# Kernel optimization log

Hardware: AMD Instinct MI355X
Metric: run time of the kernel (lower is better)

The kernel has to match this reference:

```python
import jax, jax.numpy as jnp
from jax import lax
import numpy as np

H = 32  # hidden size
I = 1   # input size

def setup_inputs() -> dict:
    key = jax.random.key(0)
    ks = jax.random.split(key, 8)
    B, T = 4096, 512
    s_ih = 1.0 / np.sqrt(H)
    inp = {
        "x": jax.random.normal(ks[0], (B, T, I), dtype=jnp.float32),
        # PyTorch LSTM params, gate order (i, f, g, o)
        "W_ih": jax.random.uniform(ks[1], (4 * H, I), dtype=jnp.float32, minval=-s_ih, maxval=s_ih),
        "W_hh": jax.random.uniform(ks[2], (4 * H, H), dtype=jnp.float32, minval=-s_ih, maxval=s_ih),
        "b_ih": jax.random.uniform(ks[3], (4 * H,), dtype=jnp.float32, minval=-s_ih, maxval=s_ih),
        "b_hh": jax.random.uniform(ks[4], (4 * H,), dtype=jnp.float32, minval=-s_ih, maxval=s_ih),
        "W_head": jax.random.uniform(ks[5], (1, H), dtype=jnp.float32, minval=-s_ih, maxval=s_ih),
        "b_head": jax.random.uniform(ks[6], (1,), dtype=jnp.float32, minval=-s_ih, maxval=s_ih),
    }
    return inp

def reference(x, W_ih, W_hh, b_ih, b_hh, W_head, b_head):
    B, T, _ = x.shape
    # Precompute input contribution to all gates: [B, T, 4H]
    x_gates = jnp.einsum('bti,gi->btg', x, W_ih) + b_ih + b_hh

    def step(carry, xg_t):  # xg_t: [B, 4H]
        h, c = carry
        gates = xg_t + h @ W_hh.T
        i, f, g, o = jnp.split(gates, 4, axis=-1)
        i = jax.nn.sigmoid(i)
        f = jax.nn.sigmoid(f)
        g = jnp.tanh(g)
        o = jax.nn.sigmoid(o)
        c = f * c + i * g
        h = o * jnp.tanh(c)
        return (h, c), None

    h0 = jnp.zeros((B, H), dtype=x.dtype)
    c0 = jnp.zeros((B, H), dtype=x.dtype)
    (h_last, _), _ = lax.scan(step, (h0, c0), jnp.swapaxes(x_gates, 0, 1))
    # head on last timestep: [B, 1]
    return h_last @ W_head.T + b_head
```

## Files before the change

### kernel.cpp

```cpp
#include <hip/hip_runtime.h>

#define HID 32
#define SEQ 512
#define WAVES_PER_BLOCK 8
#define BLOCK (WAVES_PER_BLOCK * 64)

typedef float v2f __attribute__((ext_vector_type(2)));


#define GRP(WA, WB, WC, WD, HP) \
  "v_pk_fma_f32 v[80:81], v[" WA "], " HP ", v[80:81] op_sel_hi:[1,0,1]\n\t" \
  "v_pk_fma_f32 v[82:83], v[" WC "], " HP ", v[82:83] op_sel_hi:[1,0,1]\n\t" \
  "v_pk_fma_f32 v[80:81], v[" WB "], " HP ", v[80:81] op_sel:[0,1,0] op_sel_hi:[1,1,1]\n\t" \
  "v_pk_fma_f32 v[82:83], v[" WD "], " HP ", v[82:83] op_sel:[0,1,0] op_sel_hi:[1,1,1]\n\t"

#define CLOBS \
  "v64","v65","v66","v67","v68","v69","v70","v71","v72","v73","v74","v75", \
  "v76","v77","v78","v79","v80","v81","v82","v83","v84","v85","v86","v87", \
  "v88","v89","v90","v91","v92","v93","v94","v95","v96","v97","v98","v99", \
  "v100","v101","v102","v103","v104","v105","v106","v107","v108","v109", \
  "v110","v111","v112","v113","v114","v115","v116","v117","v118","v119", \
  "v120","v121","v122","v123","v124","v125","v126","v127","v128","v129", \
  "v130","v131","v132","v133","v134","v135","v136","v137","v138","v139", \
  "v140","v141","v142","v143","v144","v145","v146","v147","v148","v149", \
  "v150","v151","v152","v153","v154","v155","v156","v157","v158","v159", \
  "v160","v161","v162","v163","v164","v165","v166","v167","v168","v169", \
  "v170","v171","v172","v173","v174","v175","v176","v177","v178","v179", \
  "v180","v181","v182","v183","v184","v185","v186","v187","v188","v189", \
  "v190","v191","v192","v193","v194","v195","v196","v197","v198","v199", \
  "v200","v201","v202","v203","v204","v205","v206","v207","v208","v209", \
  "v210","v211","v212","v213","v214","v215","v216","v217","v218","v219", \
  "v220","v221","v222","v223","v224","v225","v226","v227","v228","v229", \
  "v230","v231","v232","v233","v234","v235","v236","v237","v238","v239"

#define MAC_ASM(XA) \
    asm volatile( \
        "ds_read2_b32 v[84:85], %[xa] offset0:0 offset1:0\n\t" \
        "ds_read_b128 v[64:67],   %[hr] offset:0\n\t" \
        "ds_read_b128 v[68:71],   %[hr] offset:16\n\t" \
        "ds_read_b128 v[72:75],   %[hr] offset:32\n\t" \
        "ds_read_b128 v[76:79],   %[hr] offset:48\n\t" \
        "ds_read_b128 v[224:227], %[hr] offset:64\n\t" \
        "ds_read_b128 v[228:231], %[hr] offset:80\n\t" \
        "ds_read_b128 v[232:235], %[hr] offset:96\n\t" \
        "ds_read_b128 v[236:239], %[hr] offset:112\n\t" \
        "v_add_u32 %[xa], 4, %[xa]\n\t" \
        "s_waitcnt lgkmcnt(8)\n\t" \
        "v_pk_fma_f32 v[80:81], %[uvIF], v[84:85], %[bvIF]\n\t" \
        "v_pk_fma_f32 v[82:83], %[uvGO], v[84:85], %[bvGO]\n\t" \
        "s_waitcnt lgkmcnt(7)\n\t" \
        GRP("96:97","98:99","160:161","162:163","v[64:65]") \
        GRP("100:101","102:103","164:165","166:167","v[66:67]") \
        "s_waitcnt lgkmcnt(6)\n\t" \
        GRP("104:105","106:107","168:169","170:171","v[68:69]") \
        GRP("108:109","110:111","172:173","174:175","v[70:71]") \
        "s_waitcnt lgkmcnt(5)\n\t" \
        GRP("112:113","114:115","176:177","178:179","v[72:73]") \
        GRP("116:117","118:119","180:181","182:183","v[74:75]") \
        "s_waitcnt lgkmcnt(4)\n\t" \
        GRP("120:121","122:123","184:185","186:187","v[76:77]") \
        GRP("124:125","126:127","188:189","190:191","v[78:79]") \
        "s_waitcnt lgkmcnt(3)\n\t" \
        GRP("128:129","130:131","192:193","194:195","v[224:225]") \
        GRP("132:133","134:135","196:197","198:199","v[226:227]") \
        "s_waitcnt lgkmcnt(2)\n\t" \
        GRP("136:137","138:139","200:201","202:203","v[228:229]") \
        GRP("140:141","142:143","204:205","206:207","v[230:231]") \
        "s_waitcnt lgkmcnt(1)\n\t" \
        GRP("144:145","146:147","208:209","210:211","v[232:233]") \
        GRP("148:149","150:151","212:213","214:215","v[234:235]") \
        "s_waitcnt lgkmcnt(0)\n\t" \
        GRP("152:153","154:155","216:217","218:219","v[236:237]") \
        GRP("156:157","158:159","220:221","222:223","v[238:239]") \
        : [xa]"+v"(XA) \
        : [hr]"v"(hr), [uvIF]"v"(uvIF), [bvIF]"v"(bvIF), \
          [uvGO]"v"(uvGO), [bvGO]"v"(bvGO) \
        : "memory", CLOBS)

#define ACT_ASM() \
    asm volatile( \
        "v_mul_f32 v86, 0xbfb8aa3b, v80\n\t" \
        "v_mul_f32 v87, 0xbfb8aa3b, v81\n\t" \
        "v_mul_f32 v88, 0x4038aa3b, v82\n\t" \
        "v_mul_f32 v89, 0xbfb8aa3b, v83\n\t" \
        "v_exp_f32 v86, v86\n\t" \
        "v_exp_f32 v87, v87\n\t" \
        "v_exp_f32 v88, v88\n\t" \
        "v_exp_f32 v89, v89\n\t" \
        "v_add_f32 v86, 1.0, v86\n\t" \
        "v_add_f32 v87, 1.0, v87\n\t" \
        "v_add_f32 v88, 1.0, v88\n\t" \
        "v_add_f32 v89, 1.0, v89\n\t" \
        "v_rcp_f32 v86, v86\n\t" \
        "v_rcp_f32 v87, v87\n\t" \
        "v_rcp_f32 v88, v88\n\t" \
        "v_rcp_f32 v89, v89\n\t" \
        "s_nop 1\n\t" \
        "v_fma_f32 v90, -2.0, v88, 1.0\n\t" \
        "v_mul_f32 v91, v86, v90\n\t" \
        "v_fma_f32 %[c], v87, %[c], v91\n\t" \
        "v_mul_f32 v92, 0x4038aa3b, %[c]\n\t" \
        "v_exp_f32 v92, v92\n\t" \
        "s_nop 1\n\t" \
        "v_add_f32 v92, 1.0, v92\n\t" \
        "v_rcp_f32 v92, v92\n\t" \
        "s_nop 1\n\t" \
        "v_fma_f32 v92, -2.0, v92, 1.0\n\t" \
        "v_mul_f32 %[h], v89, v92\n\t" \
        "ds_write_b32 %[hw], %[h]\n\t" \
        : [h]"+v"(h), [c]"+v"(c) \
        : [hw]"v"(hw) \
        : "memory", CLOBS)

#define BAR() __builtin_amdgcn_s_barrier()

__global__ __launch_bounds__(BLOCK)
void lstm_fused_kernel(
    const float* __restrict__ x,
    const float* __restrict__ W_ih,
    const float* __restrict__ W_hh,
    const float* __restrict__ b_ih,
    const float* __restrict__ b_hh,
    const float* __restrict__ W_head,
    const float* __restrict__ b_head,
    float* __restrict__ out)
{
    __shared__ __align__(16) v2f WIFL[32][34];
    __shared__ __align__(16) v2f WGOL[32][34];
    __shared__ __align__(16) float Xall[WAVES_PER_BLOCK][2][SEQ];
    __shared__ __align__(16) float Hbuf[WAVES_PER_BLOCK][2][32];

    const int tid = threadIdx.x;
    for (int idx = tid; idx < 1024; idx += BLOCK) {
        const int u = idx >> 5;
        const int j = idx & 31;
        WIFL[u][j] = (v2f){ W_hh[u * 32 + j],        W_hh[(32 + u) * 32 + j] };
        WGOL[u][j] = (v2f){ W_hh[(64 + u) * 32 + j], W_hh[(96 + u) * 32 + j] };
    }
    {
        const int base = blockIdx.x * 16;
        for (int idx = tid; idx < 16 * SEQ; idx += BLOCK) {
            const int smp = idx >> 9;
            const int t   = idx & (SEQ - 1);
            Xall[smp >> 1][smp & 1][t] = x[(size_t)(base + smp) * SEQ + t];
        }
    }
    __syncthreads();

    const int lane = tid & 63;
    const int u    = lane & 31;
    const int s    = lane >> 5;
    const int wid  = tid >> 6;
    const bool even = (wid < 4);

    {
        const unsigned aIF = (unsigned)(size_t)&WIFL[u][0];
        const unsigned aGO = (unsigned)(size_t)&WGOL[u][0];
        asm volatile(
            "ds_read_b128 v[96:99],   %[wa] offset:0\n\t"
            "ds_read_b128 v[100:103], %[wa] offset:16\n\t"
            "ds_read_b128 v[104:107], %[wa] offset:32\n\t"
            "ds_read_b128 v[108:111], %[wa] offset:48\n\t"
            "ds_read_b128 v[112:115], %[wa] offset:64\n\t"
            "ds_read_b128 v[116:119], %[wa] offset:80\n\t"
            "ds_read_b128 v[120:123], %[wa] offset:96\n\t"
            "ds_read_b128 v[124:127], %[wa] offset:112\n\t"
            "ds_read_b128 v[128:131], %[wa] offset:128\n\t"
            "ds_read_b128 v[132:135], %[wa] offset:144\n\t"
            "ds_read_b128 v[136:139], %[wa] offset:160\n\t"
            "ds_read_b128 v[140:143], %[wa] offset:176\n\t"
            "ds_read_b128 v[144:147], %[wa] offset:192\n\t"
            "ds_read_b128 v[148:151], %[wa] offset:208\n\t"
            "ds_read_b128 v[152:155], %[wa] offset:224\n\t"
            "ds_read_b128 v[156:159], %[wa] offset:240\n\t"
            "ds_read_b128 v[160:163], %[wb] offset:0\n\t"
            "ds_read_b128 v[164:167], %[wb] offset:16\n\t"
            "ds_read_b128 v[168:171], %[wb] offset:32\n\t"
            "ds_read_b128 v[172:175], %[wb] offset:48\n\t"
            "ds_read_b128 v[176:179], %[wb] offset:64\n\t"
            "ds_read_b128 v[180:183], %[wb] offset:80\n\t"
            "ds_read_b128 v[184:187], %[wb] offset:96\n\t"
            "ds_read_b128 v[188:191], %[wb] offset:112\n\t"
            "ds_read_b128 v[192:195], %[wb] offset:128\n\t"
            "ds_read_b128 v[196:199], %[wb] offset:144\n\t"
            "ds_read_b128 v[200:203], %[wb] offset:160\n\t"
            "ds_read_b128 v[204:207], %[wb] offset:176\n\t"
            "ds_read_b128 v[208:211], %[wb] offset:192\n\t"
            "ds_read_b128 v[212:215], %[wb] offset:208\n\t"
            "ds_read_b128 v[216:219], %[wb] offset:224\n\t"
            "ds_read_b128 v[220:223], %[wb] offset:240\n\t"
            "s_waitcnt lgkmcnt(0)"
            :
            : [wa]"v"(aIF), [wb]"v"(aGO)
            : "memory", CLOBS);
    }

    const v2f bvIF = { b_ih[u]      + b_hh[u],      b_ih[32 + u] + b_hh[32 + u] };
    const v2f bvGO = { b_ih[64 + u] + b_hh[64 + u], b_ih[96 + u] + b_hh[96 + u] };
    const v2f uvIF = { W_ih[u],      W_ih[32 + u] };
    const v2f uvGO = { W_ih[64 + u], W_ih[96 + u] };

    const unsigned hr = (unsigned)(size_t)&Hbuf[wid][s][0];
    const unsigned hw = hr + (unsigned)(u * 4);
    unsigned xa = (unsigned)(size_t)&Xall[wid][s][0];

    float h = 0.0f, c = 0.0f;
    Hbuf[wid][s][u] = 0.0f;
    __syncthreads();

    if (even) {
        BAR();
#pragma unroll 1
        for (int t = 0; t < SEQ - 1; ++t) {
            MAC_ASM(xa);  BAR();
            ACT_ASM();    BAR();
        }
        MAC_ASM(xa);  BAR();
        ACT_ASM();
    } else {
        MAC_ASM(xa);  BAR();
#pragma unroll 1
        for (int t = 0; t < SEQ - 1; ++t) {
            ACT_ASM();    BAR();
            MAC_ASM(xa);  BAR();
        }
        ACT_ASM();  BAR();
    }

    float v = h * W_head[u];
#pragma unroll
    for (int off = 16; off >= 1; off >>= 1)
        v += __shfl_xor(v, off);
    if (u == 0) out[blockIdx.x * 16 + wid * 2 + s] = v + b_head[0];
}

extern "C" void kernel_launch(void* const* d_in, const int* in_sizes, int n_in,
                              void* d_out, int out_size, void* d_ws, size_t ws_size,
                              hipStream_t stream) {
    const float* x      = (const float*)d_in[0];
    const float* W_ih   = (const float*)d_in[1];
    const float* W_hh   = (const float*)d_in[2];
    const float* b_ih   = (const float*)d_in[3];
    const float* b_hh   = (const float*)d_in[4];
    const float* W_head = (const float*)d_in[5];
    const float* b_head = (const float*)d_in[6];
    float* out = (float*)d_out;

    const int B = in_sizes[0] / SEQ;
    const int grid = B / 16;

    lstm_fused_kernel<<<grid, BLOCK, 0, stream>>>(
        x, W_ih, W_hh, b_ih, b_hh, W_head, b_head, out);
}
```

Baseline: 316.2 us.

## Drop per-step block barriers and fuse MAC and activation into unrolled asm

Removes the lockstep barrier scheme in which half the waves ran the mat-vec while the other half ran activations. Each wave now runs its own fully fused step (LDS reads, packed FMAs, activations, h write), with the i/f exponentials interleaved into the tail of the FMA chain and s_setprio raised during the mat-vec. The loop body is unrolled 32 steps per asm block, and blocks shrink to 4 waves with twice the grid so more independent blocks share a CU. The cost is that overlap between waves now depends on the hardware scheduler instead of explicit barrier phasing. Each wave reads only the h it writes, but nothing orders an LDS write before the next step's reads other than the in-order lgkm counter.

New measurement: 278.2 us. 12.0% less time.

```diff
diff --git a/kernel.cpp b/kernel.cpp
--- a/kernel.cpp
+++ b/kernel.cpp
@@ -2,7 +2,7 @@
 
 #define HID 32
 #define SEQ 512
-#define WAVES_PER_BLOCK 8
+#define WAVES_PER_BLOCK 4
 #define BLOCK (WAVES_PER_BLOCK * 64)
 
 typedef float v2f __attribute__((ext_vector_type(2)));
@@ -13,6 +13,89 @@
   "v_pk_fma_f32 v[82:83], v[" WC "], " HP ", v[82:83] op_sel_hi:[1,0,1]\n\t" \
   "v_pk_fma_f32 v[80:81], v[" WB "], " HP ", v[80:81] op_sel:[0,1,0] op_sel_hi:[1,1,1]\n\t" \
   "v_pk_fma_f32 v[82:83], v[" WD "], " HP ", v[82:83] op_sel:[0,1,0] op_sel_hi:[1,1,1]\n\t"
+
+#define PKIF(E, O, HP) \
+  "v_pk_fma_f32 v[80:81], v[" E "], " HP ", v[80:81] op_sel_hi:[1,0,1]\n\t" \
+  "v_pk_fma_f32 v[80:81], v[" O "], " HP ", v[80:81] op_sel:[0,1,0] op_sel_hi:[1,1,1]\n\t"
+#define PKGO(E, O, HP) \
+  "v_pk_fma_f32 v[82:83], v[" E "], " HP ", v[82:83] op_sel_hi:[1,0,1]\n\t" \
+  "v_pk_fma_f32 v[82:83], v[" O "], " HP ", v[82:83] op_sel:[0,1,0] op_sel_hi:[1,1,1]\n\t"
+
+#define STEP \
+  "s_setprio 1\n\t" \
+  "ds_read2_b32 v[84:85], %[xa] offset0:0 offset1:0\n\t" \
+  "ds_read_b128 v[64:67],   %[hr] offset:0\n\t" \
+  "ds_read_b128 v[68:71],   %[hr] offset:16\n\t" \
+  "ds_read_b128 v[72:75],   %[hr] offset:32\n\t" \
+  "ds_read_b128 v[76:79],   %[hr] offset:48\n\t" \
+  "ds_read_b128 v[224:227], %[hr] offset:64\n\t" \
+  "ds_read_b128 v[228:231], %[hr] offset:80\n\t" \
+  "ds_read_b128 v[232:235], %[hr] offset:96\n\t" \
+  "ds_read_b128 v[236:239], %[hr] offset:112\n\t" \
+  "v_add_u32 %[xa], 4, %[xa]\n\t" \
+  "s_waitcnt lgkmcnt(8)\n\t" \
+  "v_pk_fma_f32 v[80:81], %[uvIF], v[84:85], %[bvIF]\n\t" \
+  "v_pk_fma_f32 v[82:83], %[uvGO], v[84:85], %[bvGO]\n\t" \
+  "s_waitcnt lgkmcnt(7)\n\t" \
+  GRP("96:97","98:99","160:161","162:163","v[64:65]") \
+  GRP("100:101","102:103","164:165","166:167","v[66:67]") \
+  "s_waitcnt lgkmcnt(6)\n\t" \
+  GRP("104:105","106:107","168:169","170:171","v[68:69]") \
+  GRP("108:109","110:111","172:173","174:175","v[70:71]") \
+  "s_waitcnt lgkmcnt(5)\n\t" \
+  GRP("112:113","114:115","176:177","178:179","v[72:73]") \
+  GRP("116:117","118:119","180:181","182:183","v[74:75]") \
+  "s_waitcnt lgkmcnt(4)\n\t" \
+  GRP("120:121","122:123","184:185","186:187","v[76:77]") \
+  GRP("124:125","126:127","188:189","190:191","v[78:79]") \
+  "s_waitcnt lgkmcnt(3)\n\t" \
+  GRP("128:129","130:131","192:193","194:195","v[224:225]") \
+  GRP("132:133","134:135","196:197","198:199","v[226:227]") \
+  "s_waitcnt lgkmcnt(2)\n\t" \
+  GRP("136:137","138:139","200:201","202:203","v[228:229]") \
+  GRP("140:141","142:143","204:205","206:207","v[230:231]") \
+  "s_waitcnt lgkmcnt(1)\n\t" \
+  GRP("144:145","146:147","208:209","210:211","v[232:233]") \
+  GRP("148:149","150:151","212:213","214:215","v[234:235]") \
+  "s_waitcnt lgkmcnt(0)\n\t" \
+   \
+  PKIF("152:153","154:155","v[236:237]") \
+  PKIF("156:157","158:159","v[238:239]") \
+  "v_mul_f32 v86, 0xbfb8aa3b, v80\n\t" \
+  "v_exp_f32 v86, v86\n\t" \
+  "v_mul_f32 v87, 0xbfb8aa3b, v81\n\t" \
+  "v_exp_f32 v87, v87\n\t" \
+  PKGO("216:217","218:219","v[236:237]") \
+  PKGO("220:221","222:223","v[238:239]") \
+  "s_setprio 0\n\t" \
+  "v_mul_f32 v88, 0x4038aa3b, v82\n\t" \
+  "v_exp_f32 v88, v88\n\t" \
+  "v_mul_f32 v89, 0xbfb8aa3b, v83\n\t" \
+  "v_exp_f32 v89, v89\n\t" \
+  "v_add_f32 v86, 1.0, v86\n\t" \
+  "v_add_f32 v87, 1.0, v87\n\t" \
+  "v_add_f32 v88, 1.0, v88\n\t" \
+  "v_add_f32 v89, 1.0, v89\n\t" \
+  "v_rcp_f32 v86, v86\n\t" \
+  "v_rcp_f32 v87, v87\n\t" \
+  "v_rcp_f32 v88, v88\n\t" \
+  "v_rcp_f32 v89, v89\n\t" \
+  "s_nop 1\n\t" \
+  "v_fma_f32 v90, -2.0, v88, 1.0\n\t" \
+  "v_mul_f32 v91, v86, v90\n\t" \
+  "v_fma_f32 %[c], v87, %[c], v91\n\t" \
+  "v_mul_f32 v92, 0x4038aa3b, %[c]\n\t" \
+  "v_exp_f32 v92, v92\n\t" \
+  "s_nop 1\n\t" \
+  "v_add_f32 v92, 1.0, v92\n\t" \
+  "v_rcp_f32 v92, v92\n\t" \
+  "s_nop 1\n\t" \
+  "v_fma_f32 v92, -2.0, v92, 1.0\n\t" \
+  "v_mul_f32 %[h], v89, v92\n\t" \
+  "ds_write_b32 %[hw], %[h]\n\t"
+
+#define S4  STEP STEP STEP STEP
+#define X32 S4 S4 S4 S4 S4 S4 S4 S4
 
 #define CLOBS \
   "v64","v65","v66","v67","v68","v69","v70","v71","v72","v73","v74","v75", \
@@ -33,87 +116,6 @@
   "v220","v221","v222","v223","v224","v225","v226","v227","v228","v229", \
   "v230","v231","v232","v233","v234","v235","v236","v237","v238","v239"
 
-#define MAC_ASM(XA) \
-    asm volatile( \
-        "ds_read2_b32 v[84:85], %[xa] offset0:0 offset1:0\n\t" \
-        "ds_read_b128 v[64:67],   %[hr] offset:0\n\t" \
-        "ds_read_b128 v[68:71],   %[hr] offset:16\n\t" \
-        "ds_read_b128 v[72:75],   %[hr] offset:32\n\t" \
-        "ds_read_b128 v[76:79],   %[hr] offset:48\n\t" \
-        "ds_read_b128 v[224:227], %[hr] offset:64\n\t" \
-        "ds_read_b128 v[228:231], %[hr] offset:80\n\t" \
-        "ds_read_b128 v[232:235], %[hr] offset:96\n\t" \
-        "ds_read_b128 v[236:239], %[hr] offset:112\n\t" \
-        "v_add_u32 %[xa], 4, %[xa]\n\t" \
-        "s_waitcnt lgkmcnt(8)\n\t" \
-        "v_pk_fma_f32 v[80:81], %[uvIF], v[84:85], %[bvIF]\n\t" \
-        "v_pk_fma_f32 v[82:83], %[uvGO], v[84:85], %[bvGO]\n\t" \
-        "s_waitcnt lgkmcnt(7)\n\t" \
-        GRP("96:97","98:99","160:161","162:163","v[64:65]") \
-        GRP("100:101","102:103","164:165","166:167","v[66:67]") \
-        "s_waitcnt lgkmcnt(6)\n\t" \
-        GRP("104:105","106:107","168:169","170:171","v[68:69]") \
-        GRP("108:109","110:111","172:173","174:175","v[70:71]") \
-        "s_waitcnt lgkmcnt(5)\n\t" \
-        GRP("112:113","114:115","176:177","178:179","v[72:73]") \
-        GRP("116:117","118:119","180:181","182:183","v[74:75]") \
-        "s_waitcnt lgkmcnt(4)\n\t" \
-        GRP("120:121","122:123","184:185","186:187","v[76:77]") \
-        GRP("124:125","126:127","188:189","190:191","v[78:79]") \
-        "s_waitcnt lgkmcnt(3)\n\t" \
-        GRP("128:129","130:131","192:193","194:195","v[224:225]") \
-        GRP("132:133","134:135","196:197","198:199","v[226:227]") \
-        "s_waitcnt lgkmcnt(2)\n\t" \
-        GRP("136:137","138:139","200:201","202:203","v[228:229]") \
-        GRP("140:141","142:143","204:205","206:207","v[230:231]") \
-        "s_waitcnt lgkmcnt(1)\n\t" \
-        GRP("144:145","146:147","208:209","210:211","v[232:233]") \
-        GRP("148:149","150:151","212:213","214:215","v[234:235]") \
-        "s_waitcnt lgkmcnt(0)\n\t" \
-        GRP("152:153","154:155","216:217","218:219","v[236:237]") \
-        GRP("156:157","158:159","220:221","222:223","v[238:239]") \
-        : [xa]"+v"(XA) \
-        : [hr]"v"(hr), [uvIF]"v"(uvIF), [bvIF]"v"(bvIF), \
-          [uvGO]"v"(uvGO), [bvGO]"v"(bvGO) \
-        : "memory", CLOBS)
-
-#define ACT_ASM() \
-    asm volatile( \
-        "v_mul_f32 v86, 0xbfb8aa3b, v80\n\t" \
-        "v_mul_f32 v87, 0xbfb8aa3b, v81\n\t" \
-        "v_mul_f32 v88, 0x4038aa3b, v82\n\t" \
-        "v_mul_f32 v89, 0xbfb8aa3b, v83\n\t" \
-        "v_exp_f32 v86, v86\n\t" \
-        "v_exp_f32 v87, v87\n\t" \
-        "v_exp_f32 v88, v88\n\t" \
-        "v_exp_f32 v89, v89\n\t" \
-        "v_add_f32 v86, 1.0, v86\n\t" \
-        "v_add_f32 v87, 1.0, v87\n\t" \
-        "v_add_f32 v88, 1.0, v88\n\t" \
-        "v_add_f32 v89, 1.0, v89\n\t" \
-        "v_rcp_f32 v86, v86\n\t" \
-        "v_rcp_f32 v87, v87\n\t" \
-        "v_rcp_f32 v88, v88\n\t" \
-        "v_rcp_f32 v89, v89\n\t" \
-        "s_nop 1\n\t" \
-        "v_fma_f32 v90, -2.0, v88, 1.0\n\t" \
-        "v_mul_f32 v91, v86, v90\n\t" \
-        "v_fma_f32 %[c], v87, %[c], v91\n\t" \
-        "v_mul_f32 v92, 0x4038aa3b, %[c]\n\t" \
-        "v_exp_f32 v92, v92\n\t" \
-        "s_nop 1\n\t" \
-        "v_add_f32 v92, 1.0, v92\n\t" \
-        "v_rcp_f32 v92, v92\n\t" \
-        "s_nop 1\n\t" \
-        "v_fma_f32 v92, -2.0, v92, 1.0\n\t" \
-        "v_mul_f32 %[h], v89, v92\n\t" \
-        "ds_write_b32 %[hw], %[h]\n\t" \
-        : [h]"+v"(h), [c]"+v"(c) \
-        : [hw]"v"(hw) \
-        : "memory", CLOBS)
-
-#define BAR() __builtin_amdgcn_s_barrier()
-
 __global__ __launch_bounds__(BLOCK)
 void lstm_fused_kernel(
     const float* __restrict__ x,
@@ -138,8 +140,8 @@
         WGOL[u][j] = (v2f){ W_hh[(64 + u) * 32 + j], W_hh[(96 + u) * 32 + j] };
     }
     {
-        const int base = blockIdx.x * 16;
-        for (int idx = tid; idx < 16 * SEQ; idx += BLOCK) {
+        const int base = blockIdx.x * 8;
+        for (int idx = tid; idx < 8 * SEQ; idx += BLOCK) {
             const int smp = idx >> 9;
             const int t   = idx & (SEQ - 1);
             Xall[smp >> 1][smp & 1][t] = x[(size_t)(base + smp) * SEQ + t];
@@ -151,7 +153,7 @@
     const int u    = lane & 31;
     const int s    = lane >> 5;
     const int wid  = tid >> 6;
-    const bool even = (wid < 4);
+    const int b0   = blockIdx.x * 8 + wid * 2;
 
     {
         const unsigned aIF = (unsigned)(size_t)&WIFL[u][0];
@@ -206,32 +208,23 @@
 
     float h = 0.0f, c = 0.0f;
     Hbuf[wid][s][u] = 0.0f;
-    __syncthreads();
-
-    if (even) {
-        BAR();
+
 #pragma unroll 1
-        for (int t = 0; t < SEQ - 1; ++t) {
-            MAC_ASM(xa);  BAR();
-            ACT_ASM();    BAR();
-        }
-        MAC_ASM(xa);  BAR();
-        ACT_ASM();
-    } else {
-        MAC_ASM(xa);  BAR();
-#pragma unroll 1
-        for (int t = 0; t < SEQ - 1; ++t) {
-            ACT_ASM();    BAR();
-            MAC_ASM(xa);  BAR();
-        }
-        ACT_ASM();  BAR();
+    for (int t0 = 0; t0 < SEQ; t0 += 32) {
+        asm volatile(
+            X32
+            : [h]"+v"(h), [c]"+v"(c), [xa]"+v"(xa)
+            : [hr]"v"(hr), [hw]"v"(hw),
+              [uvIF]"v"(uvIF), [bvIF]"v"(bvIF),
+              [uvGO]"v"(uvGO), [bvGO]"v"(bvGO)
+            : "memory", CLOBS);
     }
 
     float v = h * W_head[u];
 #pragma unroll
     for (int off = 16; off >= 1; off >>= 1)
         v += __shfl_xor(v, off);
-    if (u == 0) out[blockIdx.x * 16 + wid * 2 + s] = v + b_head[0];
+    if (u == 0) out[b0 + s] = v + b_head[0];
 }
 
 extern "C" void kernel_launch(void* const* d_in, const int* in_sizes, int n_in,
@@ -247,7 +240,7 @@
     float* out = (float*)d_out;
 
     const int B = in_sizes[0] / SEQ;
-    const int grid = B / 16;
+    const int grid = B / 8;
 
     lstm_fused_kernel<<<grid, BLOCK, 0, stream>>>(
         x, W_ih, W_hh, b_ih, b_hh, W_head, b_head, out);
```
